# Optimization experiments

Hardware: AMD Instinct MI355X
Metric: run time of the kernel (lower is better)

Reference implementation:

```python
import jax, jax.numpy as jnp
import numpy as np

ST_HIDDEN = 128
ST_HEADS = 4
ST_LAYERS = 3
RES_SCALE = 1.0
DK = ST_HIDDEN // ST_HEADS


def build_3d_adj(spatial_ei, spatial_ea, n_nodes, window):
    # replicate spatial edges per time slice with node offset t*n_nodes
    offs = (jnp.arange(window) * n_nodes)[None, :, None]  # [1,W,1]
    all_sp_idx = (spatial_ei[:, None, :] + offs).reshape(2, -1)  # [2, W*E]
    all_sp_attr = jnp.tile(spatial_ea, (window, 1))  # [W*E, De]
    # temporal edges t -> t+1 for every node
    src = jnp.arange((window - 1) * n_nodes)
    temp_idx = jnp.stack([src, src + n_nodes], axis=0)  # [2, (W-1)*N]
    temp_attr = jnp.broadcast_to(spatial_ea.mean(axis=0, keepdims=True),
                                 (temp_idx.shape[1], spatial_ea.shape[1]))
    ei = jnp.concatenate([all_sp_idx, temp_idx], axis=1)
    ea = jnp.concatenate([all_sp_attr, temp_attr], axis=0)
    return ei, ea


def seg_softmax(logits, dst, num_nodes):
    # logits [E,H], segment softmax over dst (pyg_softmax)
    m = jax.ops.segment_max(logits, dst, num_segments=num_nodes)  # [N,H]
    ex = jnp.exp(logits - m[dst])
    s = jax.ops.segment_sum(ex, dst, num_segments=num_nodes)
    return ex / (s[dst] + 1e-16)


def layernorm(x, g, b, eps=1e-5):
    mu = x.mean(-1, keepdims=True)
    var = ((x - mu) ** 2).mean(-1, keepdims=True)
    return (x - mu) * jax.lax.rsqrt(var + eps) * g + b


def block(x, ei, ea, qw, qb, kw, kb, vw, vb, fw, fb, ow, ob, ln_g, ln_b):
    B, Nt, _ = x.shape
    H, dk = ST_HEADS, DK
    Q = (x @ qw + qb).reshape(B, Nt, H, dk)
    K = (x @ kw + kb).reshape(B, Nt, H, dk)
    V = (x @ vw + vb).reshape(B, Nt, H, dk)
    src, dst = ei[0], ei[1]
    q_e = Q[:, dst]  # [B,E,H,dk]
    k_e = K[:, src]
    v_e = V[:, src]
    film = ea @ fw + fb  # [E, 2*hidden]
    gamma, beta = jnp.split(film, 2, axis=-1)
    gamma = gamma.reshape(1, -1, H, dk)
    beta = beta.reshape(1, -1, H, dk)
    k_e = k_e * (1.0 + gamma) + beta
    logits = (q_e * k_e).sum(-1) / np.sqrt(dk).astype(np.float32)  # [B,E,H]
    att = jax.vmap(lambda l: seg_softmax(l, dst, Nt))(logits)
    msg = att[..., None] * v_e  # [B,E,H,dk]
    out = jnp.zeros((B, Nt, H, dk), x.dtype).at[:, dst].add(msg)
    y = out.reshape(B, Nt, H * dk) @ ow + ob
    return layernorm(x + y, ln_g, ln_b)


def setup_inputs() -> dict:
    key = jax.random.key(0)
    ks = jax.random.split(key, 12)
    B, W, N, Fin, E, De = 2, 16, 1000, 16, 16000, 8
    H, L = ST_HIDDEN, ST_LAYERS
    g = lambda k, s: jax.random.normal(k, s, jnp.float32) * 0.05
    return {
        "xw": jax.random.normal(ks[0], (B, W, N, Fin), jnp.float32),
        "spatial_ei": jax.random.randint(ks[1], (2, E), 0, N),
        "spatial_ea": jax.random.normal(ks[2], (E, De), jnp.float32),
        "in_w": g(ks[3], (Fin, H)), "in_b": jnp.zeros((H,), jnp.float32),
        "qw": g(ks[4], (L, H, H)), "qb": jnp.zeros((L, H), jnp.float32),
        "kw": g(ks[5], (L, H, H)), "kb": jnp.zeros((L, H), jnp.float32),
        "vw": g(ks[6], (L, H, H)), "vb": jnp.zeros((L, H), jnp.float32),
        "fw": g(ks[7], (L, De, 2 * H)), "fb": jnp.zeros((L, 2 * H), jnp.float32),
        "ow": g(ks[8], (L, H, H)), "ob": jnp.zeros((L, H), jnp.float32),
        "ln_g": jnp.ones((L, H), jnp.float32), "ln_b": jnp.zeros((L, H), jnp.float32),
        "head_w": g(ks[9], (H, 1)), "head_b": jnp.zeros((1,), jnp.float32),
    }


def reference(xw, spatial_ei, spatial_ea, in_w, in_b, qw, qb, kw, kb, vw, vb,
              fw, fb, ow, ob, ln_g, ln_b, head_w, head_b):
    B, W, N, Fin = xw.shape
    ei, ea = build_3d_adj(spatial_ei, spatial_ea, N, W)
    x = xw.reshape(B, W * N, Fin) @ in_w + in_b
    for l in range(ST_LAYERS):
        bx = block(x, ei, ea, qw[l], qb[l], kw[l], kb[l], vw[l], vb[l],
                   fw[l], fb[l], ow[l], ob[l], ln_g[l], ln_b[l])
        x = x + RES_SCALE * (bx - x)
    last = x.reshape(B, W, N, -1)[:, -1]  # [B,N,H]
    return jax.nn.softplus(last @ head_w + head_b).squeeze(-1)  # [B,N]
```

## Files before the change

### kernel.cpp

```cpp
#include <hip/hip_runtime.h>
#include <math.h>

constexpr int B    = 2;
constexpr int W    = 16;
constexpr int N    = 1000;
constexpr int FIN  = 16;
constexpr int E    = 16000;
constexpr int DE   = 8;
constexpr int H    = 128;
constexpr int L    = 3;
constexpr int WL   = 4;
constexpr int W0G  = 12;
constexpr int RPB  = WL * N;
constexpr int ROWS = B * RPB;
constexpr int NMAT = 12;

__device__ __forceinline__ float dpp_add_xor1(float x) {
  int y = __builtin_amdgcn_update_dpp(0, __float_as_int(x), 0xB1, 0xF, 0xF, true);
  return x + __int_as_float(y);
}
__device__ __forceinline__ float dpp_add_xor2(float x) {
  int y = __builtin_amdgcn_update_dpp(0, __float_as_int(x), 0x4E, 0xF, 0xF, true);
  return x + __int_as_float(y);
}
__device__ __forceinline__ float headSum32(float p) {
  p = dpp_add_xor1(p);
  p = dpp_add_xor2(p);
  p += __shfl_xor(p, 4);
  p += __shfl_xor(p, 8);
  p += __shfl_xor(p, 16);
  return p;
}
__device__ __forceinline__ float dot4(float4 a, float4 b) {
  return a.x * b.x + a.y * b.y + a.z * b.z + a.w * b.w;
}

__global__ void k_hist(const int* __restrict__ ei, int* __restrict__ cnt,
                       const float* __restrict__ ea, float* __restrict__ meanea) {
  int bid = blockIdx.x;
  int t = threadIdx.x;
  if (bid < 64) {
    int e = bid * 256 + t;
    if (e < E) atomicAdd(&cnt[ei[E + e]], 1);
  } else {
    __shared__ float sbuf[256];
    int d = t & 7, g = t >> 3;
    float s = 0.f;
    for (int e = (bid - 64) * 32 + g; e < E; e += 64 * 32) s += ea[(long)e * DE + d];
    sbuf[t] = s;
    __syncthreads();
    for (int st = 16; st >= 1; st >>= 1) {
      if (g < st) sbuf[g * 8 + d] += sbuf[(g + st) * 8 + d];
      __syncthreads();
    }
    if (g == 0) atomicAdd(&meanea[d], sbuf[d]);
  }
}

__global__ void k_scan(const int* __restrict__ cnt, int* __restrict__ offs,
                       int* __restrict__ cursor) {
  __shared__ int scn[1024];
  int t = threadIdx.x;
  int v = (t < N) ? cnt[t] : 0;
  scn[t] = v;
  __syncthreads();
  for (int st = 1; st < 1024; st <<= 1) {
    int add = (t >= st) ? scn[t - st] : 0;
    __syncthreads();
    scn[t] += add;
    __syncthreads();
  }
  if (t < N) {
    offs[t + 1] = scn[t];
    if (t == 0) offs[0] = 0;
    cursor[t] = scn[t] - v;
  }
}

__global__ void k_prep2(const int* __restrict__ ei,
                        int* __restrict__ cursor, int2* __restrict__ csr,
                        const float* __restrict__ qw, const float* __restrict__ kw,
                        const float* __restrict__ vw, const float* __restrict__ ow,
                        float4* __restrict__ wTp4,
                        const float* __restrict__ xw, const float* __restrict__ in_w,
                        const float* __restrict__ in_b, float* __restrict__ x) {
  int bid = blockIdx.x;
  int t = threadIdx.x;
  if (bid < 64) {
    int e = bid * 256 + t;
    if (e < E) {
      int src = ei[e];
      int dst = ei[E + e];
      int pos = atomicAdd(&cursor[dst], 1);
      csr[pos] = make_int2(src, e);
    }
  } else if (bid < 64 + NMAT * 16) {
    int bid2 = bid - 64;
    int mat = bid2 / 16;
    int pair = bid2 % 16;
    int kk4 = pair * 2 + (t >> 7);
    int c = t & 127;
    int l = mat >> 2, mm = mat & 3;
    const float* src = ((mm == 0) ? qw : (mm == 1) ? kw : (mm == 2) ? vw : ow) + (long)l * H * H;
    int k0 = kk4 * 4;
    float4 v4;
    v4.x = src[(k0 + 0) * H + c];
    v4.y = src[(k0 + 1) * H + c];
    v4.z = src[(k0 + 2) * H + c];
    v4.w = src[(k0 + 3) * H + c];
    wTp4[((long)mat * 32 + kk4) * H + c] = v4;
  } else {
    int bi = bid - (64 + NMAT * 16);
    int b = bi / 63, tt = bi % 63;
    int lr0 = tt * 64;
    __shared__ float xwS[64][FIN];
    __shared__ float inS[FIN][H];
    for (int i = t; i < 64 * FIN; i += 256) {
      int r = i >> 4, k = i & 15;
      int lr = lr0 + r;
      float val = 0.f;
      if (lr < RPB) {
        int wl = lr / N, n = lr % N;
        val = xw[(((long)b * W + (W0G + wl)) * N + n) * FIN + k];
      }
      xwS[r][k] = val;
    }
    for (int i = t; i < FIN * H; i += 256) inS[i >> 7][i & 127] = in_w[i];
    __syncthreads();
    #pragma unroll
    for (int qi = 0; qi < 8; qi++) {
      int idx = t + qi * 256;
      int r = idx >> 5, cq = idx & 31;
      int lr = lr0 + r;
      if (lr < RPB) {
        float4 acc = *(const float4*)(in_b + cq * 4);
        #pragma unroll
        for (int k = 0; k < FIN; k++) {
          float xv = xwS[r][k];
          float4 w4 = *(const float4*)(&inS[k][cq * 4]);
          acc.x += xv * w4.x; acc.y += xv * w4.y; acc.z += xv * w4.z; acc.w += xv * w4.w;
        }
        *(float4*)(x + ((long)b * RPB + lr) * H + cq * 4) = acc;
      }
    }
  }
}

__global__ void k_gemm(const float* __restrict__ X, const float4* __restrict__ wTp4,
                       int matBase,
                       const float* __restrict__ bq, const float* __restrict__ bk,
                       const float* __restrict__ bv,
                       float* __restrict__ Cq, float* __restrict__ Ck, float* __restrict__ Cv,
                       int base, int rows_pb, int tiles) {
  int m = blockIdx.y;
  const float* bm = (m == 0) ? bq : (m == 1) ? bk : bv;
  float* Cm       = (m == 0) ? Cq : (m == 1) ? Ck : Cv;
  const float4* wp = wTp4 + (long)(matBase + m) * 32 * H;
  int bb = blockIdx.x / tiles;
  int tt = blockIdx.x % tiles;
  int lr0 = tt * 32;
  long grow0 = (long)bb * RPB + base + lr0;
  int t = threadIdx.x;
  __shared__ float xs[32][H];
  #pragma unroll
  for (int qi = 0; qi < 4; qi++) {
    int idx = t + qi * 256;
    int r = idx >> 5, c4 = idx & 31;
    float4 v4 = make_float4(0.f, 0.f, 0.f, 0.f);
    if (lr0 + r < rows_pb) v4 = *(const float4*)(X + (grow0 + r) * H + c4 * 4);
    *(float4*)&xs[r][c4 * 4] = v4;
  }
  __syncthreads();
  int cg = t & 31, rg = t >> 5;
  float4 bias4 = *(const float4*)(bm + cg * 4);
  float4 acc0 = bias4, acc1 = bias4, acc2 = bias4, acc3 = bias4;
  #pragma unroll 4
  for (int kk4 = 0; kk4 < 32; kk4++) {
    const float4* wr = wp + kk4 * H + cg * 4;
    float4 w0 = wr[0], w1 = wr[1], w2 = wr[2], w3 = wr[3];
    float4 x0 = *(const float4*)&xs[rg * 4 + 0][kk4 * 4];
    float4 x1 = *(const float4*)&xs[rg * 4 + 1][kk4 * 4];
    float4 x2 = *(const float4*)&xs[rg * 4 + 2][kk4 * 4];
    float4 x3 = *(const float4*)&xs[rg * 4 + 3][kk4 * 4];
    acc0.x += dot4(x0, w0); acc0.y += dot4(x0, w1); acc0.z += dot4(x0, w2); acc0.w += dot4(x0, w3);
    acc1.x += dot4(x1, w0); acc1.y += dot4(x1, w1); acc1.z += dot4(x1, w2); acc1.w += dot4(x1, w3);
    acc2.x += dot4(x2, w0); acc2.y += dot4(x2, w1); acc2.z += dot4(x2, w2); acc2.w += dot4(x2, w3);
    acc3.x += dot4(x3, w0); acc3.y += dot4(x3, w1); acc3.z += dot4(x3, w2); acc3.w += dot4(x3, w3);
  }
  int lrr = lr0 + rg * 4;
  if (lrr + 0 < rows_pb) *(float4*)(Cm + (grow0 + rg * 4 + 0) * H + cg * 4) = acc0;
  if (lrr + 1 < rows_pb) *(float4*)(Cm + (grow0 + rg * 4 + 1) * H + cg * 4) = acc1;
  if (lrr + 2 < rows_pb) *(float4*)(Cm + (grow0 + rg * 4 + 2) * H + cg * 4) = acc2;
  if (lrr + 3 < rows_pb) *(float4*)(Cm + (grow0 + rg * 4 + 3) * H + cg * 4) = acc3;
}

__global__ void k_attn_oln(const float* __restrict__ Qb, const float* __restrict__ Kb,
                           const float* __restrict__ Vb,
                           const float* __restrict__ ea,
                           const float* __restrict__ fw_l, const float* __restrict__ fb_l,
                           const float* __restrict__ meanea,
                           const int* __restrict__ offs, const int2* __restrict__ csr,
                           const float* __restrict__ x, const float4* __restrict__ owp,
                           const float* __restrict__ ob, const float* __restrict__ lng,
                           const float* __restrict__ lnb, float* __restrict__ xo,
                           int out_lo,
                           const float* __restrict__ hw, const float* __restrict__ hb,
                           float* __restrict__ out, int do_head) {
  int tid = threadIdx.x;
  int nwin = WL - out_lo;
  int idx = blockIdx.x;
  int b = idx / (nwin * N);
  int rem = idx % (nwin * N);
  int wl = out_lo + rem / N;
  int n = rem % N;
  long drow = ((long)b * WL + wl) * N + n;
  float q = Qb[drow * H + tid];
  long sbase = ((long)b * WL + wl) * N;
  long trow  = ((long)b * WL + wl - 1) * N + n;
  const float scale = 0.17677669529663687f;
  int i0 = offs[n], i1 = offs[n + 1];

  float rgw[DE], rbw[DE];
  #pragma unroll
  for (int d = 0; d < DE; d++) {
    rgw[d] = fw_l[d * 2 * H + tid];
    rbw[d] = fw_l[d * 2 * H + H + tid];
  }
  float fbg = fb_l[tid], fbb = fb_l[H + tid];
  const float4* eap = (const float4*)ea;

  float g = fbg, be = fbb;
  #pragma unroll
  for (int d = 0; d < DE; d++) {
    float am = meanea[d] * (1.0f / E);
    g  += am * rgw[d];
    be += am * rbw[d];
  }
  float kv = Kb[trow * H + tid];
  float vv = Vb[trow * H + tid];
  float p  = q * (kv * (1.f + g) + be);
  float pe = __expf(headSum32(p) * scale);
  float ssum = pe, acc = pe * vv;

  for (int i4 = i0; i4 < i1; i4 += 4) {
    #pragma unroll
    for (int j = 0; j < 4; j++) {
      int i = i4 + j;
      int ic = (i < i1) ? i : (i1 - 1);
      int2 se = csr[ic];
      long srow = sbase + se.x;
      float4 a0 = eap[(long)se.y * 2];
      float4 a1 = eap[(long)se.y * 2 + 1];
      float g2 = fbg + a0.x * rgw[0] + a0.y * rgw[1] + a0.z * rgw[2] + a0.w * rgw[3]
                     + a1.x * rgw[4] + a1.y * rgw[5] + a1.z * rgw[6] + a1.w * rgw[7];
      float b2 = fbb + a0.x * rbw[0] + a0.y * rbw[1] + a0.z * rbw[2] + a0.w * rbw[3]
                     + a1.x * rbw[4] + a1.y * rbw[5] + a1.z * rbw[6] + a1.w * rbw[7];
      float kv2 = Kb[srow * H + tid];
      float vv2 = Vb[srow * H + tid];
      float p2  = q * (kv2 * (1.f + g2) + b2);
      float pe2 = __expf(headSum32(p2) * scale);
      pe2 = (i < i1) ? pe2 : 0.f;
      ssum += pe2;
      acc  += pe2 * vv2;
    }
  }
  float ab = acc / (ssum + 1e-16f);

  __shared__ float sab[H];
  __shared__ float s2m[2];
  sab[tid] = ab;
  __syncthreads();
  float y = ob[tid];
  #pragma unroll 8
  for (int kk4 = 0; kk4 < 32; kk4++) {
    float4 w4 = owp[kk4 * H + tid];
    float4 a4 = *(const float4*)&sab[kk4 * 4];
    y += dot4(a4, w4);
  }

  float v = x[drow * H + tid] + y;
  float s1 = v;
  #pragma unroll
  for (int off = 32; off >= 1; off >>= 1) s1 += __shfl_xor(s1, off);
  __syncthreads();
  if ((tid & 63) == 0) s2m[tid >> 6] = s1;
  __syncthreads();
  float mu = (s2m[0] + s2m[1]) * (1.f / H);
  float dv = v - mu;
  float s2 = dv * dv;
  #pragma unroll
  for (int off = 32; off >= 1; off >>= 1) s2 += __shfl_xor(s2, off);
  __syncthreads();
  if ((tid & 63) == 0) s2m[tid >> 6] = s2;
  __syncthreads();
  float var = (s2m[0] + s2m[1]) * (1.f / H);
  float o = dv * rsqrtf(var + 1e-5f) * lng[tid] + lnb[tid];

  if (!do_head) {
    xo[drow * H + tid] = o;
  } else {
    float hv = o * hw[tid];
    #pragma unroll
    for (int off = 32; off >= 1; off >>= 1) hv += __shfl_xor(hv, off);
    __syncthreads();
    if ((tid & 63) == 0) s2m[tid >> 6] = hv;
    __syncthreads();
    if (tid == 0) {
      float z = s2m[0] + s2m[1] + hb[0];
      out[b * N + n] = fmaxf(z, 0.f) + log1pf(expf(-fabsf(z)));
    }
  }
}

extern "C" void kernel_launch(void* const* d_in, const int* in_sizes, int n_in,
                              void* d_out, int out_size, void* d_ws, size_t ws_size,
                              hipStream_t stream) {
  const float* xw   = (const float*)d_in[0];
  const int*   ei   = (const int*)d_in[1];
  const float* ea   = (const float*)d_in[2];
  const float* in_w = (const float*)d_in[3];
  const float* in_b = (const float*)d_in[4];
  const float* qw   = (const float*)d_in[5];
  const float* qb   = (const float*)d_in[6];
  const float* kw   = (const float*)d_in[7];
  const float* kb   = (const float*)d_in[8];
  const float* vw   = (const float*)d_in[9];
  const float* vb   = (const float*)d_in[10];
  const float* fw   = (const float*)d_in[11];
  const float* fb   = (const float*)d_in[12];
  const float* ow   = (const float*)d_in[13];
  const float* ob   = (const float*)d_in[14];
  const float* ln_g = (const float*)d_in[15];
  const float* ln_b = (const float*)d_in[16];
  const float* hw   = (const float*)d_in[17];
  const float* hb   = (const float*)d_in[18];
  float* out = (float*)d_out;

  float* ws   = (float*)d_ws;
  float* x    = ws;
  float* x2   = x  + (long)ROWS * H;
  float* Qb   = x2 + (long)ROWS * H;
  float* Kb   = Qb + (long)ROWS * H;
  float* Vb   = Kb + (long)ROWS * H;
  float* wTp  = Vb + (long)ROWS * H;
  int2* csr    = (int2*)(wTp + (long)NMAT * H * H);
  int* cnt     = (int*)(csr + E);
  float* meanea = (float*)(cnt + N);
  int* offs    = (int*)(meanea + 8);
  int* cursor  = offs + N + 1;
  float4* wTp4 = (float4*)wTp;

  hipMemsetAsync(cnt, 0, (N + 8) * sizeof(int), stream);
  k_hist<<<128, 256, 0, stream>>>(ei, cnt, ea, meanea);
  k_scan<<<1, 1024, 0, stream>>>(cnt, offs, cursor);
  k_prep2<<<64 + NMAT * 16 + 126, 256, 0, stream>>>(
      ei, cursor, csr, qw, kw, vw, ow, wTp4, xw, in_w, in_b, x);

  float* xa = x;
  float* xb = x2;
  for (int l = 0; l < L; l++) {
    int in_lo = l, out_lo = l + 1;
    int rows_pb = (WL - in_lo) * N;
    int tiles = (rows_pb + 31) / 32;
    k_gemm<<<dim3(B * tiles, 3), 256, 0, stream>>>(
        xa, wTp4, l * 4, qb + (long)l * H, kb + (long)l * H, vb + (long)l * H,
        Qb, Kb, Vb, in_lo * N, rows_pb, tiles);
    int nout = B * (WL - out_lo) * N;
    int last = (l == L - 1) ? 1 : 0;
    k_attn_oln<<<nout, H, 0, stream>>>(
        Qb, Kb, Vb, ea, fw + (long)l * DE * 2 * H, fb + (long)l * 2 * H, meanea,
        offs, csr,
        xa, wTp4 + ((long)l * 4 + 3) * 32 * H, ob + (long)l * H,
        ln_g + (long)l * H, ln_b + (long)l * H, xb, out_lo,
        hw, hb, out, last);
    float* tmp = xa; xa = xb; xb = tmp;
  }
}
```

Measured before the change: 253.8 us.

## Merge prep kernels, use per-block shared histograms, fuse layer-0 GEMM with CSR fill

Replaces the global-atomic histogram plus memset with per-block shared-memory histograms whose partial counts are summed inside the scan kernel, which also reduces the edge-attribute partial sums. The layer-0 QKV GEMM is folded into the same launch as the CSR scatter so both run concurrently, and the GEMM body becomes a shared device function. Together these cut the setup launch count from five to three and reduce contention on global atomics. The cost is extra partial-sum buffers and a single-block scan that now reads sixteen partial histograms.

```diff
diff --git a/kernel.cpp b/kernel.cpp
--- a/kernel.cpp
+++ b/kernel.cpp
@@ -14,6 +14,10 @@
 constexpr int RPB  = WL * N;
 constexpr int ROWS = B * RPB;
 constexpr int NMAT = 12;
+constexpr int HB   = 16;
+constexpr int EHB  = E / HB;
+constexpr int TILES0 = (RPB + 31) / 32;
+constexpr int NG0  = 3 * B * TILES0;
 
 __device__ __forceinline__ float dpp_add_xor1(float x) {
   int y = __builtin_amdgcn_update_dpp(0, __float_as_int(x), 0xB1, 0xF, 0xF, true);
@@ -35,69 +39,85 @@
   return a.x * b.x + a.y * b.y + a.z * b.z + a.w * b.w;
 }
 
-__global__ void k_hist(const int* __restrict__ ei, int* __restrict__ cnt,
-                       const float* __restrict__ ea, float* __restrict__ meanea) {
-  int bid = blockIdx.x;
+__device__ __forceinline__ void gemm_tile(
+    const float* __restrict__ X, const float4* __restrict__ wTp4, int matBase,
+    const float* __restrict__ bq, const float* __restrict__ bk,
+    const float* __restrict__ bv,
+    float* __restrict__ Cq, float* __restrict__ Ck, float* __restrict__ Cv,
+    int base, int rows_pb, int m, int bb, int tt, float xs[][H]) {
+  const float* bm = (m == 0) ? bq : (m == 1) ? bk : bv;
+  float* Cm       = (m == 0) ? Cq : (m == 1) ? Ck : Cv;
+  const float4* wp = wTp4 + (long)(matBase + m) * 32 * H;
+  int lr0 = tt * 32;
+  long grow0 = (long)bb * RPB + base + lr0;
   int t = threadIdx.x;
-  if (bid < 64) {
-    int e = bid * 256 + t;
-    if (e < E) atomicAdd(&cnt[ei[E + e]], 1);
-  } else {
-    __shared__ float sbuf[256];
-    int d = t & 7, g = t >> 3;
-    float s = 0.f;
-    for (int e = (bid - 64) * 32 + g; e < E; e += 64 * 32) s += ea[(long)e * DE + d];
-    sbuf[t] = s;
-    __syncthreads();
-    for (int st = 16; st >= 1; st >>= 1) {
-      if (g < st) sbuf[g * 8 + d] += sbuf[(g + st) * 8 + d];
-      __syncthreads();
-    }
-    if (g == 0) atomicAdd(&meanea[d], sbuf[d]);
-  }
-}
-
-__global__ void k_scan(const int* __restrict__ cnt, int* __restrict__ offs,
-                       int* __restrict__ cursor) {
-  __shared__ int scn[1024];
-  int t = threadIdx.x;
-  int v = (t < N) ? cnt[t] : 0;
-  scn[t] = v;
-  __syncthreads();
-  for (int st = 1; st < 1024; st <<= 1) {
-    int add = (t >= st) ? scn[t - st] : 0;
-    __syncthreads();
-    scn[t] += add;
-    __syncthreads();
-  }
-  if (t < N) {
-    offs[t + 1] = scn[t];
-    if (t == 0) offs[0] = 0;
-    cursor[t] = scn[t] - v;
-  }
-}
-
-__global__ void k_prep2(const int* __restrict__ ei,
-                        int* __restrict__ cursor, int2* __restrict__ csr,
+  #pragma unroll
+  for (int qi = 0; qi < 4; qi++) {
+    int idx = t + qi * 256;
+    int r = idx >> 5, c4 = idx & 31;
+    float4 v4 = make_float4(0.f, 0.f, 0.f, 0.f);
+    if (lr0 + r < rows_pb) v4 = *(const float4*)(X + (grow0 + r) * H + c4 * 4);
+    *(float4*)&xs[r][c4 * 4] = v4;
+  }
+  __syncthreads();
+  int cg = t & 31, rg = t >> 5;
+  float4 bias4 = *(const float4*)(bm + cg * 4);
+  float4 acc0 = bias4, acc1 = bias4, acc2 = bias4, acc3 = bias4;
+  #pragma unroll 4
+  for (int kk4 = 0; kk4 < 32; kk4++) {
+    const float4* wr = wp + kk4 * H + cg * 4;
+    float4 w0 = wr[0], w1 = wr[1], w2 = wr[2], w3 = wr[3];
+    float4 x0 = *(const float4*)&xs[rg * 4 + 0][kk4 * 4];
+    float4 x1 = *(const float4*)&xs[rg * 4 + 1][kk4 * 4];
+    float4 x2 = *(const float4*)&xs[rg * 4 + 2][kk4 * 4];
+    float4 x3 = *(const float4*)&xs[rg * 4 + 3][kk4 * 4];
+    acc0.x += dot4(x0, w0); acc0.y += dot4(x0, w1); acc0.z += dot4(x0, w2); acc0.w += dot4(x0, w3);
+    acc1.x += dot4(x1, w0); acc1.y += dot4(x1, w1); acc1.z += dot4(x1, w2); acc1.w += dot4(x1, w3);
+    acc2.x += dot4(x2, w0); acc2.y += dot4(x2, w1); acc2.z += dot4(x2, w2); acc2.w += dot4(x2, w3);
+    acc3.x += dot4(x3, w0); acc3.y += dot4(x3, w1); acc3.z += dot4(x3, w2); acc3.w += dot4(x3, w3);
+  }
+  int lrr = lr0 + rg * 4;
+  if (lrr + 0 < rows_pb) *(float4*)(Cm + (grow0 + rg * 4 + 0) * H + cg * 4) = acc0;
+  if (lrr + 1 < rows_pb) *(float4*)(Cm + (grow0 + rg * 4 + 1) * H + cg * 4) = acc1;
+  if (lrr + 2 < rows_pb) *(float4*)(Cm + (grow0 + rg * 4 + 2) * H + cg * 4) = acc2;
+  if (lrr + 3 < rows_pb) *(float4*)(Cm + (grow0 + rg * 4 + 3) * H + cg * 4) = acc3;
+}
+
+__global__ void k_prepA(const int* __restrict__ ei, const float* __restrict__ ea,
+                        int* __restrict__ cnt_part, float* __restrict__ easum_part,
                         const float* __restrict__ qw, const float* __restrict__ kw,
                         const float* __restrict__ vw, const float* __restrict__ ow,
                         float4* __restrict__ wTp4,
                         const float* __restrict__ xw, const float* __restrict__ in_w,
                         const float* __restrict__ in_b, float* __restrict__ x) {
+  __shared__ float xwS[64][FIN];
+  __shared__ float inS[FIN][H];
   int bid = blockIdx.x;
   int t = threadIdx.x;
-  if (bid < 64) {
-    int e = bid * 256 + t;
-    if (e < E) {
-      int src = ei[e];
-      int dst = ei[E + e];
-      int pos = atomicAdd(&cursor[dst], 1);
-      csr[pos] = make_int2(src, e);
-    }
-  } else if (bid < 64 + NMAT * 16) {
-    int bid2 = bid - 64;
-    int mat = bid2 / 16;
-    int pair = bid2 % 16;
+  if (bid < HB) {
+    int* hcnt = (int*)&xwS[0][0];
+    for (int i = t; i < 1024; i += 256) hcnt[i] = 0;
+    __syncthreads();
+    int e0 = bid * EHB;
+    for (int e = e0 + t; e < e0 + EHB; e += 256) atomicAdd(&hcnt[ei[E + e]], 1);
+    __syncthreads();
+    for (int i = t; i < 1024; i += 256) cnt_part[bid * 1024 + i] = hcnt[i];
+  } else if (bid < HB + 64) {
+    float* sbuf = &inS[0][0];
+    int u = bid - HB;
+    int d = t & 7, g = t >> 3;
+    float s = 0.f;
+    for (int e = u * 32 + g; e < E; e += 64 * 32) s += ea[(long)e * DE + d];
+    sbuf[t] = s;
+    __syncthreads();
+    for (int st = 16; st >= 1; st >>= 1) {
+      if (g < st) sbuf[g * 8 + d] += sbuf[(g + st) * 8 + d];
+      __syncthreads();
+    }
+    if (g == 0) easum_part[u * 8 + d] = sbuf[d];
+  } else if (bid < HB + 64 + NMAT * 16) {
+    int u = bid - (HB + 64);
+    int mat = u / 16, pair = u % 16;
     int kk4 = pair * 2 + (t >> 7);
     int c = t & 127;
     int l = mat >> 2, mm = mat & 3;
@@ -110,11 +130,9 @@
     v4.w = src[(k0 + 3) * H + c];
     wTp4[((long)mat * 32 + kk4) * H + c] = v4;
   } else {
-    int bi = bid - (64 + NMAT * 16);
-    int b = bi / 63, tt = bi % 63;
+    int u = bid - (HB + 64 + NMAT * 16);
+    int b = u / 63, tt = u % 63;
     int lr0 = tt * 64;
-    __shared__ float xwS[64][FIN];
-    __shared__ float inS[FIN][H];
     for (int i = t; i < 64 * FIN; i += 256) {
       int r = i >> 4, k = i & 15;
       int lr = lr0 + r;
@@ -146,52 +164,70 @@
   }
 }
 
+__global__ void k_scan2(const int* __restrict__ cnt_part,
+                        const float* __restrict__ easum_part,
+                        int* __restrict__ offs, int* __restrict__ cursor,
+                        float* __restrict__ meanea) {
+  __shared__ int scn[1024];
+  int t = threadIdx.x;
+  int v = 0;
+  #pragma unroll
+  for (int b = 0; b < HB; b++) v += cnt_part[b * 1024 + t];
+  scn[t] = v;
+  __syncthreads();
+  for (int st = 1; st < 1024; st <<= 1) {
+    int add = (t >= st) ? scn[t - st] : 0;
+    __syncthreads();
+    scn[t] += add;
+    __syncthreads();
+  }
+  if (t < N) {
+    offs[t + 1] = scn[t];
+    if (t == 0) offs[0] = 0;
+    cursor[t] = scn[t] - v;
+  }
+  if (t < 8) {
+    float s = 0.f;
+    for (int i = 0; i < 64; i++) s += easum_part[i * 8 + t];
+    meanea[t] = s;
+  }
+}
+
+__global__ void k_g0csr(const float* __restrict__ X, const float4* __restrict__ wTp4,
+                        const float* __restrict__ bq, const float* __restrict__ bk,
+                        const float* __restrict__ bv,
+                        float* __restrict__ Cq, float* __restrict__ Ck,
+                        float* __restrict__ Cv,
+                        const int* __restrict__ ei, int* __restrict__ cursor,
+                        int2* __restrict__ csr) {
+  __shared__ float xs[32][H];
+  int bid = blockIdx.x;
+  int t = threadIdx.x;
+  if (bid < NG0) {
+    int m = bid / (B * TILES0);
+    int rest = bid % (B * TILES0);
+    int bb = rest / TILES0, tt = rest % TILES0;
+    gemm_tile(X, wTp4, 0, bq, bk, bv, Cq, Ck, Cv, 0, RPB, m, bb, tt, xs);
+  } else {
+    int e = (bid - NG0) * 256 + t;
+    if (e < E) {
+      int sr = ei[e];
+      int d  = ei[E + e];
+      int pos = atomicAdd(&cursor[d], 1);
+      csr[pos] = make_int2(sr, e);
+    }
+  }
+}
+
 __global__ void k_gemm(const float* __restrict__ X, const float4* __restrict__ wTp4,
                        int matBase,
                        const float* __restrict__ bq, const float* __restrict__ bk,
                        const float* __restrict__ bv,
                        float* __restrict__ Cq, float* __restrict__ Ck, float* __restrict__ Cv,
                        int base, int rows_pb, int tiles) {
-  int m = blockIdx.y;
-  const float* bm = (m == 0) ? bq : (m == 1) ? bk : bv;
-  float* Cm       = (m == 0) ? Cq : (m == 1) ? Ck : Cv;
-  const float4* wp = wTp4 + (long)(matBase + m) * 32 * H;
-  int bb = blockIdx.x / tiles;
-  int tt = blockIdx.x % tiles;
-  int lr0 = tt * 32;
-  long grow0 = (long)bb * RPB + base + lr0;
-  int t = threadIdx.x;
   __shared__ float xs[32][H];
-  #pragma unroll
-  for (int qi = 0; qi < 4; qi++) {
-    int idx = t + qi * 256;
-    int r = idx >> 5, c4 = idx & 31;
-    float4 v4 = make_float4(0.f, 0.f, 0.f, 0.f);
-    if (lr0 + r < rows_pb) v4 = *(const float4*)(X + (grow0 + r) * H + c4 * 4);
-    *(float4*)&xs[r][c4 * 4] = v4;
-  }
-  __syncthreads();
-  int cg = t & 31, rg = t >> 5;
-  float4 bias4 = *(const float4*)(bm + cg * 4);
-  float4 acc0 = bias4, acc1 = bias4, acc2 = bias4, acc3 = bias4;
-  #pragma unroll 4
-  for (int kk4 = 0; kk4 < 32; kk4++) {
-    const float4* wr = wp + kk4 * H + cg * 4;
-    float4 w0 = wr[0], w1 = wr[1], w2 = wr[2], w3 = wr[3];
-    float4 x0 = *(const float4*)&xs[rg * 4 + 0][kk4 * 4];
-    float4 x1 = *(const float4*)&xs[rg * 4 + 1][kk4 * 4];
-    float4 x2 = *(const float4*)&xs[rg * 4 + 2][kk4 * 4];
-    float4 x3 = *(const float4*)&xs[rg * 4 + 3][kk4 * 4];
-    acc0.x += dot4(x0, w0); acc0.y += dot4(x0, w1); acc0.z += dot4(x0, w2); acc0.w += dot4(x0, w3);
-    acc1.x += dot4(x1, w0); acc1.y += dot4(x1, w1); acc1.z += dot4(x1, w2); acc1.w += dot4(x1, w3);
-    acc2.x += dot4(x2, w0); acc2.y += dot4(x2, w1); acc2.z += dot4(x2, w2); acc2.w += dot4(x2, w3);
-    acc3.x += dot4(x3, w0); acc3.y += dot4(x3, w1); acc3.z += dot4(x3, w2); acc3.w += dot4(x3, w3);
-  }
-  int lrr = lr0 + rg * 4;
-  if (lrr + 0 < rows_pb) *(float4*)(Cm + (grow0 + rg * 4 + 0) * H + cg * 4) = acc0;
-  if (lrr + 1 < rows_pb) *(float4*)(Cm + (grow0 + rg * 4 + 1) * H + cg * 4) = acc1;
-  if (lrr + 2 < rows_pb) *(float4*)(Cm + (grow0 + rg * 4 + 2) * H + cg * 4) = acc2;
-  if (lrr + 3 < rows_pb) *(float4*)(Cm + (grow0 + rg * 4 + 3) * H + cg * 4) = acc3;
+  gemm_tile(X, wTp4, matBase, bq, bk, bv, Cq, Ck, Cv, base, rows_pb,
+            blockIdx.y, blockIdx.x / tiles, blockIdx.x % tiles, xs);
 }
 
 __global__ void k_attn_oln(const float* __restrict__ Qb, const float* __restrict__ Kb,
@@ -344,27 +380,30 @@
   float* Vb   = Kb + (long)ROWS * H;
   float* wTp  = Vb + (long)ROWS * H;
   int2* csr    = (int2*)(wTp + (long)NMAT * H * H);
-  int* cnt     = (int*)(csr + E);
-  float* meanea = (float*)(cnt + N);
+  int* cnt_part = (int*)(csr + E);
+  float* easum_part = (float*)(cnt_part + HB * 1024);
+  float* meanea = easum_part + 64 * 8;
   int* offs    = (int*)(meanea + 8);
   int* cursor  = offs + N + 1;
   float4* wTp4 = (float4*)wTp;
 
-  hipMemsetAsync(cnt, 0, (N + 8) * sizeof(int), stream);
-  k_hist<<<128, 256, 0, stream>>>(ei, cnt, ea, meanea);
-  k_scan<<<1, 1024, 0, stream>>>(cnt, offs, cursor);
-  k_prep2<<<64 + NMAT * 16 + 126, 256, 0, stream>>>(
-      ei, cursor, csr, qw, kw, vw, ow, wTp4, xw, in_w, in_b, x);
+  k_prepA<<<HB + 64 + NMAT * 16 + 126, 256, 0, stream>>>(
+      ei, ea, cnt_part, easum_part, qw, kw, vw, ow, wTp4, xw, in_w, in_b, x);
+  k_scan2<<<1, 1024, 0, stream>>>(cnt_part, easum_part, offs, cursor, meanea);
+  k_g0csr<<<NG0 + 64, 256, 0, stream>>>(
+      x, wTp4, qb, kb, vb, Qb, Kb, Vb, ei, cursor, csr);
 
   float* xa = x;
   float* xb = x2;
   for (int l = 0; l < L; l++) {
-    int in_lo = l, out_lo = l + 1;
-    int rows_pb = (WL - in_lo) * N;
-    int tiles = (rows_pb + 31) / 32;
-    k_gemm<<<dim3(B * tiles, 3), 256, 0, stream>>>(
-        xa, wTp4, l * 4, qb + (long)l * H, kb + (long)l * H, vb + (long)l * H,
-        Qb, Kb, Vb, in_lo * N, rows_pb, tiles);
+    if (l > 0) {
+      int rows_pb = (WL - l) * N;
+      int tiles = (rows_pb + 31) / 32;
+      k_gemm<<<dim3(B * tiles, 3), 256, 0, stream>>>(
+          xa, wTp4, l * 4, qb + (long)l * H, kb + (long)l * H, vb + (long)l * H,
+          Qb, Kb, Vb, l * N, rows_pb, tiles);
+    }
+    int out_lo = l + 1;
     int nout = B * (WL - out_lo) * N;
     int last = (l == L - 1) ? 1 : 0;
     k_attn_oln<<<nout, H, 0, stream>>>(
```

After: 248.5 us. 1.02x faster.
